# Kernel optimization log

Measured on AMD Instinct MI355X. Metric: run time of the kernel, lower is better.

The kernel has to match this reference:

```python
import jax, jax.numpy as jnp
import numpy as np

B, S, D_IN, D_OUT = 8, 4096, 512, 64

def setup_inputs() -> dict:
    key = jax.random.key(0)
    k1, k2, k3, k4 = jax.random.split(key, 4)
    scale = 1.0 / np.sqrt(D_IN)
    return {
        "x": jax.random.normal(k1, (B, S, D_IN), dtype=jnp.float32),
        "W_Q": jax.random.normal(k2, (D_IN, D_OUT), dtype=jnp.float32) * scale,
        "W_K": jax.random.normal(k3, (D_IN, D_OUT), dtype=jnp.float32) * scale,
        "W_V": jax.random.normal(k4, (D_IN, D_OUT), dtype=jnp.float32) * scale,
    }

def reference(x, W_Q, W_K, W_V):
    # q,k,v: [B,S,D_OUT]
    q = jnp.einsum("bsd,de->bse", x, W_Q)
    k = jnp.einsum("bsd,de->bse", x, W_K)
    v = jnp.einsum("bsd,de->bse", x, W_V)
    d_out = k.shape[-1]
    # scores: [B,S,S], causal mask (upper triangle -> -inf)
    scores = jnp.einsum("bqe,bke->bqk", q, k)
    s = q.shape[1]
    causal = jnp.tril(jnp.ones((s, s), dtype=bool))
    scores = jnp.where(causal[None, :, :], scores, -jnp.inf)
    attn = jax.nn.softmax(scores / jnp.sqrt(jnp.asarray(d_out, scores.dtype)), axis=-1)
    # dropout p=0.0 (eval) -> identity
    return jnp.einsum("bqk,bke->bqe", attn, v)
```

## Files before the change

kernel.cpp:

```cpp
#include <hip/hip_runtime.h>
#include <hip/hip_bf16.h>

#define B_    8
#define S_    4096
#define DIN   512
#define DOUT  64
#define NROWS (B_ * S_)

typedef __attribute__((ext_vector_type(8)))  short bf16x8;
typedef __attribute__((ext_vector_type(4)))  float f32x4;
typedef __attribute__((ext_vector_type(16))) float f32x16;
typedef __attribute__((ext_vector_type(2)))  unsigned int u32x2;
typedef __attribute__((ext_vector_type(2)))  int i32x2;

typedef const __attribute__((address_space(1))) unsigned int GUI;
typedef __attribute__((address_space(3))) unsigned int LUI;

__device__ __forceinline__ unsigned short f32_to_bf16(float f) {
    union { float f; unsigned int u; } c; c.f = f;
    unsigned int r = (c.u + 0x7FFFu + ((c.u >> 16) & 1u)) >> 16;
    return (unsigned short)r;
}
__device__ __forceinline__ float bf16_to_f32(unsigned short us) {
    union { unsigned int u; float f; } c; c.u = (unsigned int)us << 16;
    return c.f;
}

__device__ __forceinline__ float fast_exp2(float x) {
#if __has_builtin(__builtin_amdgcn_exp2f)
    return __builtin_amdgcn_exp2f(x);
#else
    return exp2f(x);
#endif
}

__device__ __forceinline__ float sum_xor32(float v) {
    i32x2 r = __builtin_amdgcn_permlane32_swap(__float_as_int(v), __float_as_int(v),
                                               false, false);
    return __int_as_float(r.x) + __int_as_float(r.y);
}

#define LDS_READS_DONE_FENCE() do {                                   \
    asm volatile("s_waitcnt lgkmcnt(0)" ::: "memory");                \
    __builtin_amdgcn_sched_barrier(0);                                \
} while (0)

__device__ __forceinline__ int pidx_of(int tp, int j) {
    if (tp < 16) return tp - 8;
    if (tp < 24) return 8 + (tp - 16) * 2 + (j - 1);
    return 24 + (tp - 24) * 3 + (j - 1);
}

#define PART_STRIDE 16896

__global__ void wt_convert(const float* __restrict__ WQ,
                           const float* __restrict__ WK,
                           const float* __restrict__ WV,
                           unsigned short* __restrict__ Wt2) {
    int idx = blockIdx.x * 256 + threadIdx.x;
    if (idx >= 3 * 512 * 16) return;
    int p   = idx / 8192;
    int rem = idx - p * 8192;
    int k   = rem >> 4;
    int n0  = (rem & 15) * 4;
    const float* W = (p == 0) ? WQ : ((p == 1) ? WK : WV);
    float4 v = *(const float4*)(W + k * 64 + n0);
    const int ks = k >> 5, kl = k & 31;
    float vv[4] = {v.x, v.y, v.z, v.w};
#pragma unroll
    for (int r = 0; r < 4; ++r) {
        int n = n0 + r;
        Wt2[(size_t)((ks * 12 + p * 4 + (n >> 4)) * 512) + (n & 15) * 32 + kl] =
            f32_to_bf16(vv[r]);
    }
}

__global__ __launch_bounds__(256) void qkv_proj(const float* __restrict__ x,
                                                const unsigned short* __restrict__ Wt2,
                                                unsigned short* __restrict__ QKV) {
    __shared__ alignas(16) float          xtile[2][1024];
    __shared__ alignas(16) unsigned short btile[2][6144];

    const int tid  = threadIdx.x;
    const int lane = tid & 63;
    const int wq   = tid >> 6;
    const int c15  = lane & 15;
    const int g    = lane >> 4;
    const float* xblk = x + (size_t)blockIdx.x * 32 * DIN;

    const int rw     = (wq & 1) * 16 + c15;
    const int nfbase = (wq >> 1) * 6;

    const int xrow = wq * 8 + (lane >> 3);
    const int xsl  = (lane & 7) ^ (xrow & 7);

    auto stage = [&](int slot, int ks) {
        __builtin_amdgcn_global_load_lds((GUI*)(xblk + ks * 32 + xrow * DIN + xsl * 4),
                                         (LUI*)((char*)&xtile[slot][0] + wq * 1024), 16, 0, 0);
        const unsigned short* Bs = Wt2 + (size_t)ks * 6144;
#pragma unroll
        for (int j = 0; j < 3; ++j)
            __builtin_amdgcn_global_load_lds((GUI*)(Bs + (j * 256 + tid) * 8),
                                             (LUI*)((char*)&btile[slot][0] + j * 4096 + wq * 1024),
                                             16, 0, 0);
    };
    stage(0, 0);
    stage(1, 1);

    f32x4 acc[6] = {};

    int cur = 0;
    for (int ks = 0; ks < 16; ++ks) {
        asm volatile("s_waitcnt vmcnt(4)" ::: "memory");
        asm volatile("s_barrier" ::: "memory");

        const char* xb = (const char*)&xtile[cur][0] + rw * 128;
        f32x4 a0 = *(const f32x4*)(xb + (((2 * g)     ^ (rw & 7)) << 4));
        f32x4 a1 = *(const f32x4*)(xb + (((2 * g + 1) ^ (rw & 7)) << 4));
        union { unsigned w[4]; bf16x8 v; } af;
        asm("v_cvt_pk_bf16_f32 %0, %1, %2" : "=v"(af.w[0]) : "v"(a0[0]), "v"(a0[1]));
        asm("v_cvt_pk_bf16_f32 %0, %1, %2" : "=v"(af.w[1]) : "v"(a0[2]), "v"(a0[3]));
        asm("v_cvt_pk_bf16_f32 %0, %1, %2" : "=v"(af.w[2]) : "v"(a1[0]), "v"(a1[1]));
        asm("v_cvt_pk_bf16_f32 %0, %1, %2" : "=v"(af.w[3]) : "v"(a1[2]), "v"(a1[3]));

        const char* bb = (const char*)&btile[cur][0] + c15 * 64 + g * 16;
#pragma unroll
        for (int n = 0; n < 6; ++n) {
            bf16x8 bf = *(const bf16x8*)(bb + (nfbase + n) * 1024);
            acc[n] = __builtin_amdgcn_mfma_f32_16x16x32_bf16(af.v, bf, acc[n], 0, 0, 0);
        }

        LDS_READS_DONE_FENCE();
        asm volatile("s_barrier" ::: "memory");
        {
            int tn = ks + 2; if (tn > 15) tn = 15;
            stage(cur, tn);
        }
        cur ^= 1;
    }
    asm volatile("s_waitcnt vmcnt(0)" ::: "memory");

    const int orow0 = blockIdx.x * 32 + (wq & 1) * 16 + g * 4;
#pragma unroll
    for (int n = 0; n < 6; ++n) {
        const int nfg  = nfbase + n;
        const int p    = nfg >> 2;
        const int ncol = (nfg & 3) * 16 + c15;
        if (p < 2) {
            unsigned short* outp = QKV + (size_t)p * NROWS * DOUT;
            const float sc = (p == 0) ? 0.125f * 1.44269504089f : 1.0f;
#pragma unroll
            for (int r = 0; r < 4; ++r)
                outp[(size_t)(orow0 + r) * DOUT + ncol] = f32_to_bf16(acc[n][r] * sc);
        } else {
            const int bb2  = orow0 >> 12;
            const int srow = orow0 & 4095;
            union { unsigned short s[4]; u32x2 d; } pk;
#pragma unroll
            for (int r = 0; r < 4; ++r) pk.s[r] = f32_to_bf16(acc[n][r]);
            *(u32x2*)(QKV + (size_t)2 * NROWS * DOUT +
                      ((size_t)bb2 * DOUT + ncol) * S_ + srow) = pk.d;
        }
    }
}

__global__ __launch_bounds__(512) void qk_norms(const unsigned short* __restrict__ QKV,
                                                float* __restrict__ qn,
                                                float* __restrict__ ktm) {
    __shared__ float lds[64];
    const int bid  = blockIdx.x;
    const bool isK = bid >= 512;
    const int blk  = isK ? bid - 512 : bid;
    const int tid  = threadIdx.x;
    const int rowl = tid >> 3;
    const int part = tid & 7;
    const size_t row = (size_t)blk * 64 + rowl;

    const unsigned short* src = QKV + (isK ? (size_t)NROWS * DOUT : 0) +
                                row * DOUT + part * 8;
    bf16x8 v = *(const bf16x8*)src;
    float s = 0.f;
#pragma unroll
    for (int i2 = 0; i2 < 8; ++i2) {
        float f = bf16_to_f32((unsigned short)v[i2]);
        s += f * f;
    }
    s += __shfl_xor(s, 1, 64);
    s += __shfl_xor(s, 2, 64);
    s += __shfl_xor(s, 4, 64);

    if (!isK) {
        if (part == 0) qn[row] = sqrtf(s);
    } else {
        if (part == 0) lds[rowl] = s;
        __syncthreads();
        if (tid < 64) {
            float m = lds[tid];
#pragma unroll
            for (int st = 32; st >= 1; st >>= 1)
                m = fmaxf(m, __shfl_xor(m, st, 64));
            if (tid == 0) ktm[blk] = sqrtf(m);
        }
    }
}

__global__ void kpref(const float* __restrict__ ktm, float* __restrict__ pm) {
    const int b = blockIdx.x;
    const int t = threadIdx.x;
    float m = 0.f;
    for (int u = 0; u <= t; ++u) m = fmaxf(m, ktm[b * 64 + u]);
    pm[b * 64 + t] = m;
}

__global__ __launch_bounds__(128) void attn_fwd(const unsigned short* __restrict__ QKV,
                                                const float* __restrict__ qn,
                                                const float* __restrict__ pm,
                                                float* __restrict__ out,
                                                char* __restrict__ part1,
                                                float* __restrict__ ml0) {
    __shared__ alignas(16) unsigned short k_lds[2][4096];
    __shared__ alignas(16) unsigned short v_lds[2][4096];

    const int bid  = blockIdx.x;
    const int b    = bid & 7;
    const int idx  = bid >> 3;
    const int half = idx & 1;
    const int i    = 79 - (idx >> 1);
    int tp, j;
    if      (i < 8)  { tp = i;                   j = 0; }
    else if (i < 24) { tp = 8 + ((i - 8) >> 1);  j = (i - 8) & 1; }
    else if (i < 48) { tp = 16 + (i - 24) / 3;   j = (i - 24) % 3; }
    else             { tp = 24 + ((i - 48) >> 2); j = (i - 48) & 3; }
    const int tile_lo  = 16 * j;
    const int tile_hi  = min(16 * j + 15, 2 * tp + 1);
    const int tile_cnt = tile_hi - tile_lo + 1;

    const int tid  = threadIdx.x;
    const int lane = tid & 63;
    const int wq   = tid >> 6;
    const int q31  = lane & 31;
    const int h    = lane >> 5;
    const int swz  = q31 & 7;
    const int rb0  = q31 * 128;

    const unsigned short* Qg  = QKV + (size_t)b * S_ * DOUT;
    const unsigned short* Kg  = QKV + (size_t)NROWS * DOUT + (size_t)b * S_ * DOUT;
    const unsigned short* VTg = QKV + (size_t)2 * NROWS * DOUT + (size_t)b * DOUT * S_;

    const int ql128 = half * 64 + wq * 32 + q31;
    const int qrow  = tp * 128 + ql128;
    const unsigned short* Qr = Qg + (size_t)qrow * DOUT + 8 * h;
    bf16x8 qf[4];
#pragma unroll
    for (int s = 0; s < 4; ++s) qf[s] = *(const bf16x8*)(Qr + 16 * s);

    const float M_r = qn[(size_t)b * S_ + qrow] * pm[b * 64 + (qrow >> 6)];
    asm volatile("s_waitcnt vmcnt(0)" ::: "memory");

    auto stage = [&](int slot, int tg) {
        const unsigned short* Kt = Kg + (size_t)tg * 64 * DOUT;
        const unsigned short* Vt = VTg + tg * 64;
#pragma unroll
        for (int r = 0; r < 4; ++r) {
            const int i2  = r * 128 + tid;
            const int row = i2 >> 3, sl = (i2 & 7) ^ (row & 7);
            __builtin_amdgcn_global_load_lds((GUI*)(Kt + row * DOUT + sl * 8),
                (LUI*)((char*)&k_lds[slot][0] + r * 2048 + wq * 1024), 16, 0, 0);
        }
#pragma unroll
        for (int r = 0; r < 4; ++r) {
            const int i2  = r * 128 + tid;
            const int row = i2 >> 3, sl = (i2 & 7) ^ (row & 7);
            __builtin_amdgcn_global_load_lds((GUI*)(Vt + (size_t)row * S_ + sl * 8),
                (LUI*)((char*)&v_lds[slot][0] + r * 2048 + wq * 1024), 16, 0, 0);
        }
    };

    stage(0, tile_lo);
    stage(1, tile_lo + 1);

    f32x16 oacc0 = {}, oacc1 = {};
    float l_r = 0.f;

    int cur = 0;
    for (int itl = 0; itl < tile_cnt; ++itl) {
        const int tg = tile_lo + itl;
        asm volatile("s_waitcnt vmcnt(8)" ::: "memory");
        asm volatile("s_barrier" ::: "memory");

        const char* kb_ = (const char*)&k_lds[cur][0];
        const char* vb_ = (const char*)&v_lds[cur][0];

        f32x16 sA = {}, sB = {};
        __builtin_amdgcn_s_setprio(1);
#pragma unroll
        for (int s = 0; s < 4; ++s) {
            const int sl = ((2 * s + h) ^ swz) << 4;
            bf16x8 ka  = *(const bf16x8*)(kb_ + rb0 + sl);
            bf16x8 kb2 = *(const bf16x8*)(kb_ + rb0 + 4096 + sl);
            sA = __builtin_amdgcn_mfma_f32_32x32x16_bf16(ka,  qf[s], sA, 0, 0, 0);
            sB = __builtin_amdgcn_mfma_f32_32x32x16_bf16(kb2, qf[s], sB, 0, 0, 0);
        }
        __builtin_amdgcn_s_setprio(0);

        if (tg >= 2 * tp) {
#pragma unroll
            for (int r2 = 0; r2 < 16; ++r2) {
                const int kvg = 64 * tg + (r2 & 3) + 8 * (r2 >> 2) + 4 * h;
                if (kvg      > qrow) sA[r2] = -1.0e30f;
                if (kvg + 32 > qrow) sB[r2] = -1.0e30f;
            }
        }

        float t0 = 0.f, t1 = 0.f, t2 = 0.f, t3 = 0.f;
#pragma unroll
        for (int k2 = 0; k2 < 16; ++k2) {
            sA[k2] = fast_exp2(sA[k2] - M_r);
            sB[k2] = fast_exp2(sB[k2] - M_r);
        }
#pragma unroll
        for (int k2 = 0; k2 < 4; ++k2) {
            t0 += sA[k2];      t1 += sA[k2 + 4];
            t0 += sA[k2 + 8];  t1 += sA[k2 + 12];
            t2 += sB[k2];      t3 += sB[k2 + 4];
            t2 += sB[k2 + 8];  t3 += sB[k2 + 12];
        }
        l_r += (t0 + t1) + (t2 + t3);

#define STEP_PV(u, Pv) do {                                                        \
        const int e0 = 2 * ((u) & 1);                                              \
        unsigned pa, pb2, pc, pd;                                                  \
        asm("v_cvt_pk_bf16_f32 %0, %1, %2" : "=v"(pa)  : "v"(Pv[4*e0+0]), "v"(Pv[4*e0+1])); \
        asm("v_cvt_pk_bf16_f32 %0, %1, %2" : "=v"(pb2) : "v"(Pv[4*e0+2]), "v"(Pv[4*e0+3])); \
        asm("v_cvt_pk_bf16_f32 %0, %1, %2" : "=v"(pc)  : "v"(Pv[4*e0+4]), "v"(Pv[4*e0+5])); \
        asm("v_cvt_pk_bf16_f32 %0, %1, %2" : "=v"(pd)  : "v"(Pv[4*e0+6]), "v"(Pv[4*e0+7])); \
        i32x2 ra = __builtin_amdgcn_permlane32_swap((int)pa,  (int)pc, false, false); \
        i32x2 rb = __builtin_amdgcn_permlane32_swap((int)pb2, (int)pd, false, false); \
        union { unsigned w[4]; bf16x8 v; } pw;                                     \
        pw.w[0] = (unsigned)ra.x; pw.w[1] = (unsigned)rb.x;                        \
        pw.w[2] = (unsigned)ra.y; pw.w[3] = (unsigned)rb.y;                        \
        const int slv = ((2 * (u) + h) ^ swz) << 4;                                \
        bf16x8 vfa = *(const bf16x8*)(vb_ + rb0 + slv);                            \
        bf16x8 vfb = *(const bf16x8*)(vb_ + rb0 + 4096 + slv);                     \
        oacc0 = __builtin_amdgcn_mfma_f32_32x32x16_bf16(vfa, pw.v, oacc0, 0, 0, 0);\
        oacc1 = __builtin_amdgcn_mfma_f32_32x32x16_bf16(vfb, pw.v, oacc1, 0, 0, 0);\
    } while (0)

        __builtin_amdgcn_s_setprio(1);
        STEP_PV(0, sA); STEP_PV(1, sA); STEP_PV(2, sB); STEP_PV(3, sB);
        __builtin_amdgcn_s_setprio(0);
#undef STEP_PV

        LDS_READS_DONE_FENCE();
        asm volatile("s_barrier" ::: "memory");
        {
            int tn = itl + 2; if (tn >= tile_cnt) tn = tile_cnt - 1;
            stage(cur, tile_lo + tn);
        }
        cur ^= 1;
    }

    asm volatile("s_waitcnt vmcnt(0)" ::: "memory");

    l_r = sum_xor32(l_r);

    if (j == 0 && tp < 8) {
        const float linv = 1.0f / l_r;
        float* op = out + (size_t)b * S_ * DOUT + (size_t)qrow * DOUT;
#pragma unroll
        for (int e = 0; e < 4; ++e) {
            f32x4 v0 = { oacc0[4*e+0]*linv, oacc0[4*e+1]*linv, oacc0[4*e+2]*linv, oacc0[4*e+3]*linv };
            f32x4 v1 = { oacc1[4*e+0]*linv, oacc1[4*e+1]*linv, oacc1[4*e+2]*linv, oacc1[4*e+3]*linv };
            *(f32x4*)(op + 8*e + 4*h)      = v0;
            *(f32x4*)(op + 32 + 8*e + 4*h) = v1;
        }
    } else if (j == 0) {
        float* op = out + (size_t)b * S_ * DOUT + (size_t)qrow * DOUT;
#pragma unroll
        for (int e = 0; e < 4; ++e) {
            f32x4 v0 = { oacc0[4*e+0], oacc0[4*e+1], oacc0[4*e+2], oacc0[4*e+3] };
            f32x4 v1 = { oacc1[4*e+0], oacc1[4*e+1], oacc1[4*e+2], oacc1[4*e+3] };
            *(f32x4*)(op + 8*e + 4*h)      = v0;
            *(f32x4*)(op + 32 + 8*e + 4*h) = v1;
        }
        if (h == 0) ml0[(size_t)(b * 24 + (tp - 8)) * 128 + ql128] = l_r;
    } else {
        char* pb_ = part1 + (size_t)(b * 48 + pidx_of(tp, j)) * PART_STRIDE;
        if (h == 0) ((float*)pb_)[ql128] = l_r;
        unsigned short* ob = (unsigned short*)(pb_ + 512);
#pragma unroll
        for (int e = 0; e < 4; ++e) {
            union { unsigned short s[4]; u32x2 d; } k0, k1;
#pragma unroll
            for (int c = 0; c < 4; ++c) { k0.s[c] = f32_to_bf16(oacc0[4*e+c]);
                                          k1.s[c] = f32_to_bf16(oacc1[4*e+c]); }
            *(u32x2*)(ob + (size_t)ql128 * 64 + 8*e + 4*h)      = k0.d;
            *(u32x2*)(ob + (size_t)ql128 * 64 + 32 + 8*e + 4*h) = k1.d;
        }
    }
}

template<int NC>
__device__ __forceinline__ void reduce_body(int b, int tp, int q, int d,
                                            float* __restrict__ out,
                                            const char* __restrict__ part1,
                                            const float* __restrict__ ml0) {
    float* otile = out + ((size_t)b * S_ + (size_t)tp * 128) * 64;
    float L = ml0[(size_t)(b * 24 + (tp - 8)) * 128 + q];
    float O = otile[(size_t)q * 64 + d];
#pragma unroll
    for (int jj = 0; jj < NC - 1; ++jj) {
        const char* pb = part1 + (size_t)(b * 48 + pidx_of(tp, jj + 1)) * PART_STRIDE;
        L += ((const float*)pb)[q];
        O += bf16_to_f32(((const unsigned short*)(pb + 512))[(size_t)q * 64 + d]);
    }
    otile[(size_t)q * 64 + d] = O / L;
}

__global__ __launch_bounds__(256) void attn_reduce(float* __restrict__ out,
                                                   const char* __restrict__ part1,
                                                   const float* __restrict__ ml0) {
    const int bid = blockIdx.x;
    const int sub = bid & 31;
    const int tz  = (bid >> 5) % 24;
    const int b   = bid / (32 * 24);
    const int tp  = tz + 8;
    const int q   = sub * 4 + (threadIdx.x >> 6);
    const int d   = threadIdx.x & 63;

    if (tp < 16)      reduce_body<2>(b, tp, q, d, out, part1, ml0);
    else if (tp < 24) reduce_body<3>(b, tp, q, d, out, part1, ml0);
    else              reduce_body<4>(b, tp, q, d, out, part1, ml0);
}

extern "C" void kernel_launch(void* const* d_in, const int* in_sizes, int n_in,
                              void* d_out, int out_size, void* d_ws, size_t ws_size,
                              hipStream_t stream) {
    const float* x  = (const float*)d_in[0];
    const float* WQ = (const float*)d_in[1];
    const float* WK = (const float*)d_in[2];
    const float* WV = (const float*)d_in[3];

    unsigned short* Wt2   = (unsigned short*)d_ws;
    unsigned short* QKV   = Wt2 + 192 * 512;
    char*           part1 = (char*)d_ws + 12779520;
    float*          ml0   = (float*)((char*)d_ws + 19267584);
    float*          qn    = (float*)((char*)d_ws + 19365888);
    float*          ktm   = (float*)((char*)d_ws + 19496960);
    float*          pmb   = (float*)((char*)d_ws + 19499008);
    float* out = (float*)d_out;

    wt_convert<<<96, 256, 0, stream>>>(WQ, WK, WV, Wt2);
    qkv_proj<<<1024, 256, 0, stream>>>(x, Wt2, QKV);
    qk_norms<<<1024, 512, 0, stream>>>(QKV, qn, ktm);
    kpref<<<8, 64, 0, stream>>>(ktm, pmb);
    attn_fwd<<<1280, 128, 0, stream>>>(QKV, qn, pmb, out, part1, ml0);
    attn_reduce<<<6144, 256, 0, stream>>>(out, part1, ml0);
}
```

Baseline: 88.42 us.

## Use single-wave attention blocks with 32-key tiles and blocked V layout

The projection kernel now writes V in a blocked layout: 32-key blocks, 8-key sub-slots, 64 columns each. This lets each 32-key V tile be loaded as a contiguous 4 KB chunk instead of strided transposed rows. The attention kernel becomes one wave per block with 32-key tiles, which removes the s_barrier syncs. Causal work is trimmed per 32-query wave, so each wave stops at its own diagonal key block. Half-size tiles double the loop iterations and the per-iteration overhead, and K/V loads are no longer shared between the two waves that used to share a block.

```diff
diff --git a/kernel.cpp b/kernel.cpp
--- a/kernel.cpp
+++ b/kernel.cpp
@@ -155,11 +155,13 @@
         } else {
             const int bb2  = orow0 >> 12;
             const int srow = orow0 & 4095;
+            const int kb   = srow >> 5;
+            const int kvl  = srow & 31;
             union { unsigned short s[4]; u32x2 d; } pk;
 #pragma unroll
             for (int r = 0; r < 4; ++r) pk.s[r] = f32_to_bf16(acc[n][r]);
-            *(u32x2*)(QKV + (size_t)2 * NROWS * DOUT +
-                      ((size_t)bb2 * DOUT + ncol) * S_ + srow) = pk.d;
+            *(u32x2*)(QKV + (size_t)2 * NROWS * DOUT + (size_t)bb2 * S_ * DOUT +
+                      ((size_t)(kb * 4 + (kvl >> 3)) * 64 + ncol) * 8 + (kvl & 7)) = pk.d;
         }
     }
 }
@@ -212,42 +214,38 @@
     pm[b * 64 + t] = m;
 }
 
-__global__ __launch_bounds__(128) void attn_fwd(const unsigned short* __restrict__ QKV,
-                                                const float* __restrict__ qn,
-                                                const float* __restrict__ pm,
-                                                float* __restrict__ out,
-                                                char* __restrict__ part1,
-                                                float* __restrict__ ml0) {
-    __shared__ alignas(16) unsigned short k_lds[2][4096];
-    __shared__ alignas(16) unsigned short v_lds[2][4096];
-
-    const int bid  = blockIdx.x;
-    const int b    = bid & 7;
-    const int idx  = bid >> 3;
-    const int half = idx & 1;
-    const int i    = 79 - (idx >> 1);
+__global__ __launch_bounds__(64) void attn_fwd(const unsigned short* __restrict__ QKV,
+                                               const float* __restrict__ qn,
+                                               const float* __restrict__ pm,
+                                               float* __restrict__ out,
+                                               char* __restrict__ part1,
+                                               float* __restrict__ ml0) {
+    __shared__ alignas(16) unsigned short k_lds[2][2048];
+    __shared__ alignas(16) unsigned short v_lds[2][2048];
+
+    const int bid = blockIdx.x;
+    const int b   = bid & 7;
+    const int w   = bid >> 3;
+    const int qq  = w & 3;
+    const int i   = 79 - (w >> 2);
     int tp, j;
     if      (i < 8)  { tp = i;                   j = 0; }
     else if (i < 24) { tp = 8 + ((i - 8) >> 1);  j = (i - 8) & 1; }
     else if (i < 48) { tp = 16 + (i - 24) / 3;   j = (i - 24) % 3; }
     else             { tp = 24 + ((i - 48) >> 2); j = (i - 48) & 3; }
-    const int tile_lo  = 16 * j;
-    const int tile_hi  = min(16 * j + 15, 2 * tp + 1);
-    const int tile_cnt = tile_hi - tile_lo + 1;
-
-    const int tid  = threadIdx.x;
-    const int lane = tid & 63;
-    const int wq   = tid >> 6;
+    const int tile_hi = min(16 * j + 15, 2 * tp + 1);
+    const int kb_lo   = 32 * j;
+    const int kb_end  = min(2 * tile_hi + 1, 4 * tp + qq);
+
+    const int lane = threadIdx.x;
     const int q31  = lane & 31;
     const int h    = lane >> 5;
-    const int swz  = q31 & 7;
-    const int rb0  = q31 * 128;
 
     const unsigned short* Qg  = QKV + (size_t)b * S_ * DOUT;
     const unsigned short* Kg  = QKV + (size_t)NROWS * DOUT + (size_t)b * S_ * DOUT;
-    const unsigned short* VTg = QKV + (size_t)2 * NROWS * DOUT + (size_t)b * DOUT * S_;
-
-    const int ql128 = half * 64 + wq * 32 + q31;
+    const unsigned short* V2g = QKV + (size_t)2 * NROWS * DOUT + (size_t)b * S_ * DOUT;
+
+    const int ql128 = qq * 32 + q31;
     const int qrow  = tp * 128 + ql128;
     const unsigned short* Qr = Qg + (size_t)qrow * DOUT + 8 * h;
     bf16x8 qf[4];
@@ -257,106 +255,88 @@
     const float M_r = qn[(size_t)b * S_ + qrow] * pm[b * 64 + (qrow >> 6)];
     asm volatile("s_waitcnt vmcnt(0)" ::: "memory");
 
-    auto stage = [&](int slot, int tg) {
-        const unsigned short* Kt = Kg + (size_t)tg * 64 * DOUT;
-        const unsigned short* Vt = VTg + tg * 64;
+    const int krow = lane >> 3;
+    auto stage = [&](int slot, int kb) {
+        const unsigned short* Kt = Kg + (size_t)kb * 2048;
+        const unsigned short* Vt = V2g + (size_t)kb * 2048;
+        char* kbase = (char*)&k_lds[slot][0];
+        char* vbase = (char*)&v_lds[slot][0];
 #pragma unroll
         for (int r = 0; r < 4; ++r) {
-            const int i2  = r * 128 + tid;
-            const int row = i2 >> 3, sl = (i2 & 7) ^ (row & 7);
+            const int row = r * 8 + krow;
+            const int sl  = (lane & 7) ^ (row & 7);
             __builtin_amdgcn_global_load_lds((GUI*)(Kt + row * DOUT + sl * 8),
-                (LUI*)((char*)&k_lds[slot][0] + r * 2048 + wq * 1024), 16, 0, 0);
-        }
-#pragma unroll
-        for (int r = 0; r < 4; ++r) {
-            const int i2  = r * 128 + tid;
-            const int row = i2 >> 3, sl = (i2 & 7) ^ (row & 7);
-            __builtin_amdgcn_global_load_lds((GUI*)(Vt + (size_t)row * S_ + sl * 8),
-                (LUI*)((char*)&v_lds[slot][0] + r * 2048 + wq * 1024), 16, 0, 0);
-        }
+                                             (LUI*)(kbase + r * 1024), 16, 0, 0);
+        }
+#pragma unroll
+        for (int r = 0; r < 4; ++r)
+            __builtin_amdgcn_global_load_lds((GUI*)(Vt + (r * 64 + lane) * 8),
+                                             (LUI*)(vbase + r * 1024), 16, 0, 0);
     };
 
-    stage(0, tile_lo);
-    stage(1, tile_lo + 1);
+    stage(0, kb_lo);
+    stage(1, min(kb_lo + 1, kb_end));
 
     f32x16 oacc0 = {}, oacc1 = {};
     float l_r = 0.f;
 
     int cur = 0;
-    for (int itl = 0; itl < tile_cnt; ++itl) {
-        const int tg = tile_lo + itl;
+    for (int kb = kb_lo; kb <= kb_end; ++kb) {
         asm volatile("s_waitcnt vmcnt(8)" ::: "memory");
-        asm volatile("s_barrier" ::: "memory");
 
         const char* kb_ = (const char*)&k_lds[cur][0];
         const char* vb_ = (const char*)&v_lds[cur][0];
 
-        f32x16 sA = {}, sB = {};
+        f32x16 sA = {};
         __builtin_amdgcn_s_setprio(1);
 #pragma unroll
         for (int s = 0; s < 4; ++s) {
-            const int sl = ((2 * s + h) ^ swz) << 4;
-            bf16x8 ka  = *(const bf16x8*)(kb_ + rb0 + sl);
-            bf16x8 kb2 = *(const bf16x8*)(kb_ + rb0 + 4096 + sl);
-            sA = __builtin_amdgcn_mfma_f32_32x32x16_bf16(ka,  qf[s], sA, 0, 0, 0);
-            sB = __builtin_amdgcn_mfma_f32_32x32x16_bf16(kb2, qf[s], sB, 0, 0, 0);
+            bf16x8 ka = *(const bf16x8*)(kb_ + q31 * 128 + (((2 * s + h) ^ (q31 & 7)) << 4));
+            sA = __builtin_amdgcn_mfma_f32_32x32x16_bf16(ka, qf[s], sA, 0, 0, 0);
         }
         __builtin_amdgcn_s_setprio(0);
 
-        if (tg >= 2 * tp) {
+        if (kb >= 4 * tp + qq) {
 #pragma unroll
             for (int r2 = 0; r2 < 16; ++r2) {
-                const int kvg = 64 * tg + (r2 & 3) + 8 * (r2 >> 2) + 4 * h;
-                if (kvg      > qrow) sA[r2] = -1.0e30f;
-                if (kvg + 32 > qrow) sB[r2] = -1.0e30f;
+                const int kvg = 32 * kb + (r2 & 3) + 8 * (r2 >> 2) + 4 * h;
+                if (kvg > qrow) sA[r2] = -1.0e30f;
             }
         }
 
-        float t0 = 0.f, t1 = 0.f, t2 = 0.f, t3 = 0.f;
-#pragma unroll
-        for (int k2 = 0; k2 < 16; ++k2) {
-            sA[k2] = fast_exp2(sA[k2] - M_r);
-            sB[k2] = fast_exp2(sB[k2] - M_r);
-        }
-#pragma unroll
-        for (int k2 = 0; k2 < 4; ++k2) {
-            t0 += sA[k2];      t1 += sA[k2 + 4];
-            t0 += sA[k2 + 8];  t1 += sA[k2 + 12];
-            t2 += sB[k2];      t3 += sB[k2 + 4];
-            t2 += sB[k2 + 8];  t3 += sB[k2 + 12];
-        }
-        l_r += (t0 + t1) + (t2 + t3);
-
-#define STEP_PV(u, Pv) do {                                                        \
-        const int e0 = 2 * ((u) & 1);                                              \
+        float t0 = 0.f, t1 = 0.f;
+#pragma unroll
+        for (int k2 = 0; k2 < 16; ++k2) sA[k2] = fast_exp2(sA[k2] - M_r);
+#pragma unroll
+        for (int k2 = 0; k2 < 8; ++k2) { t0 += sA[k2]; t1 += sA[k2 + 8]; }
+        l_r += t0 + t1;
+
+#define STEP_PV(u) do {                                                            \
+        const int e0 = 2 * (u);                                                    \
         unsigned pa, pb2, pc, pd;                                                  \
-        asm("v_cvt_pk_bf16_f32 %0, %1, %2" : "=v"(pa)  : "v"(Pv[4*e0+0]), "v"(Pv[4*e0+1])); \
-        asm("v_cvt_pk_bf16_f32 %0, %1, %2" : "=v"(pb2) : "v"(Pv[4*e0+2]), "v"(Pv[4*e0+3])); \
-        asm("v_cvt_pk_bf16_f32 %0, %1, %2" : "=v"(pc)  : "v"(Pv[4*e0+4]), "v"(Pv[4*e0+5])); \
-        asm("v_cvt_pk_bf16_f32 %0, %1, %2" : "=v"(pd)  : "v"(Pv[4*e0+6]), "v"(Pv[4*e0+7])); \
+        asm("v_cvt_pk_bf16_f32 %0, %1, %2" : "=v"(pa)  : "v"(sA[4*e0+0]), "v"(sA[4*e0+1])); \
+        asm("v_cvt_pk_bf16_f32 %0, %1, %2" : "=v"(pb2) : "v"(sA[4*e0+2]), "v"(sA[4*e0+3])); \
+        asm("v_cvt_pk_bf16_f32 %0, %1, %2" : "=v"(pc)  : "v"(sA[4*e0+4]), "v"(sA[4*e0+5])); \
+        asm("v_cvt_pk_bf16_f32 %0, %1, %2" : "=v"(pd)  : "v"(sA[4*e0+6]), "v"(sA[4*e0+7])); \
         i32x2 ra = __builtin_amdgcn_permlane32_swap((int)pa,  (int)pc, false, false); \
         i32x2 rb = __builtin_amdgcn_permlane32_swap((int)pb2, (int)pd, false, false); \
-        union { unsigned w[4]; bf16x8 v; } pw;                                     \
-        pw.w[0] = (unsigned)ra.x; pw.w[1] = (unsigned)rb.x;                        \
-        pw.w[2] = (unsigned)ra.y; pw.w[3] = (unsigned)rb.y;                        \
-        const int slv = ((2 * (u) + h) ^ swz) << 4;                                \
-        bf16x8 vfa = *(const bf16x8*)(vb_ + rb0 + slv);                            \
-        bf16x8 vfb = *(const bf16x8*)(vb_ + rb0 + 4096 + slv);                     \
+        union { unsigned wv[4]; bf16x8 v; } pw;                                    \
+        pw.wv[0] = (unsigned)ra.x; pw.wv[1] = (unsigned)rb.x;                      \
+        pw.wv[2] = (unsigned)ra.y; pw.wv[3] = (unsigned)rb.y;                      \
+        const int slot = 2 * (u) + h;                                              \
+        bf16x8 vfa = *(const bf16x8*)(vb_ + slot * 1024 + q31 * 16);               \
+        bf16x8 vfb = *(const bf16x8*)(vb_ + slot * 1024 + (32 + q31) * 16);        \
         oacc0 = __builtin_amdgcn_mfma_f32_32x32x16_bf16(vfa, pw.v, oacc0, 0, 0, 0);\
         oacc1 = __builtin_amdgcn_mfma_f32_32x32x16_bf16(vfb, pw.v, oacc1, 0, 0, 0);\
     } while (0)
 
         __builtin_amdgcn_s_setprio(1);
-        STEP_PV(0, sA); STEP_PV(1, sA); STEP_PV(2, sB); STEP_PV(3, sB);
+        STEP_PV(0); STEP_PV(1);
         __builtin_amdgcn_s_setprio(0);
 #undef STEP_PV
 
         LDS_READS_DONE_FENCE();
-        asm volatile("s_barrier" ::: "memory");
-        {
-            int tn = itl + 2; if (tn >= tile_cnt) tn = tile_cnt - 1;
-            stage(cur, tile_lo + tn);
-        }
+        stage(cur, min(kb + 2, kb_end));
         cur ^= 1;
     }
 
@@ -454,6 +434,6 @@
     qkv_proj<<<1024, 256, 0, stream>>>(x, Wt2, QKV);
     qk_norms<<<1024, 512, 0, stream>>>(QKV, qn, ktm);
     kpref<<<8, 64, 0, stream>>>(ktm, pmb);
-    attn_fwd<<<1280, 128, 0, stream>>>(QKV, qn, pmb, out, part1, ml0);
+    attn_fwd<<<2560, 64, 0, stream>>>(QKV, qn, pmb, out, part1, ml0);
     attn_reduce<<<6144, 256, 0, stream>>>(out, part1, ml0);
 }
```

Result: faster. 78.77 us (-10.9%).
